# Optimization experiments

Measured on AMD Instinct MI355X. Metric: run time of the kernel, lower is better.

## Reference

```python
import jax, jax.numpy as jnp
import numpy as np

N, E = 50000, 800000
D_IN, H, D_OUT = 64, 64, 32
NEG_SLOPE = 0.2


def setup_inputs() -> dict:
    key = jax.random.key(0)
    ks = jax.random.split(key, 20)
    inp = {
        "x": jax.random.normal(ks[0], (N, D_IN), dtype=jnp.float32),
        "edge_index": jax.random.randint(ks[1], (2, E), 0, N, dtype=jnp.int32),
    }
    def lin(k, fan_in, fan_out):
        s = 1.0 / np.sqrt(fan_in)
        return jax.random.uniform(k, (fan_in, fan_out), jnp.float32, -s, s)
    # GAT layer params: W [in,H], att_src [H], att_dst [H], bias [H]
    dims_in = [D_IN, H, H]
    for i in range(3):
        inp[f"W{i+1}"] = lin(ks[2 + 4 * i], dims_in[i], H)
        inp[f"a_src{i+1}"] = jax.random.normal(ks[3 + 4 * i], (H,), jnp.float32) * 0.1
        inp[f"a_dst{i+1}"] = jax.random.normal(ks[4 + 4 * i], (H,), jnp.float32) * 0.1
        inp[f"b{i+1}"] = jnp.zeros((H,), jnp.float32)
    inp["lin1_W"] = lin(ks[14], H, H)
    inp["lin1_b"] = jnp.zeros((H,), jnp.float32)
    inp["lin2_W"] = lin(ks[15], H, D_OUT)
    inp["lin2_b"] = jnp.zeros((D_OUT,), jnp.float32)
    return inp


def gat_layer(x, src, dst, W, a_src, a_dst, b):
    h = x @ W                                   # [N, H]
    alpha_s = (h * a_src).sum(-1)               # [N]
    alpha_d = (h * a_dst).sum(-1)               # [N]
    e = jax.nn.leaky_relu(alpha_s[src] + alpha_d[dst], NEG_SLOPE)  # [E]
    m = jax.lax.stop_gradient(jax.ops.segment_max(e, dst, num_segments=N))
    w = jnp.exp(e - m[dst])                     # [E]
    denom = jax.ops.segment_sum(w, dst, num_segments=N)
    alpha = w / denom[dst]                      # segment softmax over incoming edges
    out = jax.ops.segment_sum(alpha[:, None] * h[src], dst, num_segments=N)
    return out + b


def reference(x, edge_index, W1, a_src1, a_dst1, b1, W2, a_src2, a_dst2, b2,
              W3, a_src3, a_dst3, b3, lin1_W, lin1_b, lin2_W, lin2_b):
    src, dst = edge_index[0], edge_index[1]
    h = jax.nn.relu(gat_layer(x, src, dst, W1, a_src1, a_dst1, b1))
    h = jax.nn.relu(gat_layer(h, src, dst, W2, a_src2, a_dst2, b2))
    h = jax.nn.relu(gat_layer(h, src, dst, W3, a_src3, a_dst3, b3))
    h = jax.nn.relu(h @ lin1_W + lin1_b)
    return h @ lin2_W + lin2_b
```

## Files before the change

### kernel.cpp

```cpp
#include <hip/hip_runtime.h>

#define NEG_SLOPE 0.2f
#define NBUCK 256

template <bool WANT_ALPHA, bool DO_HIST>
__global__ __launch_bounds__(256) void gemm64(
    const float* __restrict__ x, const float* __restrict__ W,
    const float* __restrict__ a_src, const float* __restrict__ a_dst,
    float* __restrict__ out, float* __restrict__ alpha_s,
    float* __restrict__ alpha_d, int N,
    const int* __restrict__ ei, int E, int* __restrict__ bhist)
{
    __shared__ float Xs[64][68];
    __shared__ float Ws[64][64];
    __shared__ int   hsh[NBUCK];

    const int row0 = blockIdx.x * 64;

    for (int i = threadIdx.x; i < 1024; i += 256)
        ((float4*)Ws)[i] = ((const float4*)W)[i];
    for (int i = threadIdx.x; i < 1024; i += 256) {
        int r = i >> 4, c4 = (i & 15) * 4;
        float4 v = {0.f, 0.f, 0.f, 0.f};
        if (row0 + r < N) v = *(const float4*)&x[(size_t)(row0 + r) * 64 + c4];
        *(float4*)&Xs[r][c4] = v;
    }
    if (DO_HIST && blockIdx.x < 256) hsh[threadIdx.x] = 0;
    __syncthreads();

    const int tx = threadIdx.x & 15;
    const int ty = threadIdx.x >> 4;

    float acc[4][4] = {{0.f,0.f,0.f,0.f},{0.f,0.f,0.f,0.f},
                       {0.f,0.f,0.f,0.f},{0.f,0.f,0.f,0.f}};

#pragma unroll 8
    for (int k = 0; k < 64; ++k) {
        const float4 wv = *(const float4*)&Ws[k][tx * 4];
        const float x0 = Xs[ty * 4 + 0][k];
        const float x1 = Xs[ty * 4 + 1][k];
        const float x2 = Xs[ty * 4 + 2][k];
        const float x3 = Xs[ty * 4 + 3][k];
        acc[0][0] += x0 * wv.x; acc[0][1] += x0 * wv.y;
        acc[0][2] += x0 * wv.z; acc[0][3] += x0 * wv.w;
        acc[1][0] += x1 * wv.x; acc[1][1] += x1 * wv.y;
        acc[1][2] += x1 * wv.z; acc[1][3] += x1 * wv.w;
        acc[2][0] += x2 * wv.x; acc[2][1] += x2 * wv.y;
        acc[2][2] += x2 * wv.z; acc[2][3] += x2 * wv.w;
        acc[3][0] += x3 * wv.x; acc[3][1] += x3 * wv.y;
        acc[3][2] += x3 * wv.z; acc[3][3] += x3 * wv.w;
    }

#pragma unroll
    for (int i = 0; i < 4; ++i) {
        const int r = row0 + ty * 4 + i;
        if (r < N) {
            float4 o = {acc[i][0], acc[i][1], acc[i][2], acc[i][3]};
            *(float4*)&out[(size_t)r * 64 + tx * 4] = o;
        }
    }

    if (WANT_ALPHA) {
        const float4 asv = *(const float4*)&a_src[tx * 4];
        const float4 adv = *(const float4*)&a_dst[tx * 4];
#pragma unroll
        for (int i = 0; i < 4; ++i) {
            float s = acc[i][0]*asv.x + acc[i][1]*asv.y
                    + acc[i][2]*asv.z + acc[i][3]*asv.w;
            float d = acc[i][0]*adv.x + acc[i][1]*adv.y
                    + acc[i][2]*adv.z + acc[i][3]*adv.w;
#pragma unroll
            for (int off = 1; off < 16; off <<= 1) {
                s += __shfl_xor(s, off, 16);
                d += __shfl_xor(d, off, 16);
            }
            const int r = row0 + ty * 4 + i;
            if (tx == 0 && r < N) { alpha_s[r] = s; alpha_d[r] = d; }
        }
    }

    if (DO_HIST && blockIdx.x < 256) {
        __syncthreads();
        for (int e = blockIdx.x * 256 + threadIdx.x; e < E; e += 256 * 256)
            atomicAdd(&hsh[((unsigned)ei[E + e]) >> 8], 1);
        __syncthreads();
        if (hsh[threadIdx.x]) atomicAdd(&bhist[threadIdx.x], hsh[threadIdx.x]);
    }
}

__global__ __launch_bounds__(256) void gemm_head(
    const float* __restrict__ X, const float* __restrict__ W1,
    const float* __restrict__ b1, const float* __restrict__ W2,
    const float* __restrict__ b2, float* __restrict__ out, int N)
{
    __shared__ float Xs[64][68];
    __shared__ float W1s[64][64];
    __shared__ float W2s[64][32];

    const int row0 = blockIdx.x * 64;

    for (int i = threadIdx.x; i < 1024; i += 256)
        ((float4*)W1s)[i] = ((const float4*)W1)[i];
    for (int i = threadIdx.x; i < 512; i += 256)
        ((float4*)W2s)[i] = ((const float4*)W2)[i];
    for (int i = threadIdx.x; i < 1024; i += 256) {
        int r = i >> 4, c4 = (i & 15) * 4;
        float4 v = {0.f, 0.f, 0.f, 0.f};
        if (row0 + r < N) v = *(const float4*)&X[(size_t)(row0 + r) * 64 + c4];
        *(float4*)&Xs[r][c4] = v;
    }
    __syncthreads();

    const int tx = threadIdx.x & 15;
    const int ty = threadIdx.x >> 4;

    float acc[4][4] = {{0,0,0,0},{0,0,0,0},{0,0,0,0},{0,0,0,0}};
#pragma unroll 8
    for (int k = 0; k < 64; ++k) {
        const float4 wv = *(const float4*)&W1s[k][tx * 4];
        const float x0 = Xs[ty * 4 + 0][k];
        const float x1 = Xs[ty * 4 + 1][k];
        const float x2 = Xs[ty * 4 + 2][k];
        const float x3 = Xs[ty * 4 + 3][k];
        acc[0][0] += x0 * wv.x; acc[0][1] += x0 * wv.y;
        acc[0][2] += x0 * wv.z; acc[0][3] += x0 * wv.w;
        acc[1][0] += x1 * wv.x; acc[1][1] += x1 * wv.y;
        acc[1][2] += x1 * wv.z; acc[1][3] += x1 * wv.w;
        acc[2][0] += x2 * wv.x; acc[2][1] += x2 * wv.y;
        acc[2][2] += x2 * wv.z; acc[2][3] += x2 * wv.w;
        acc[3][0] += x3 * wv.x; acc[3][1] += x3 * wv.y;
        acc[3][2] += x3 * wv.z; acc[3][3] += x3 * wv.w;
    }

    const float4 bv = *(const float4*)&b1[tx * 4];
    __syncthreads();
#pragma unroll
    for (int i = 0; i < 4; ++i) {
        Xs[ty * 4 + i][tx * 4 + 0] = fmaxf(acc[i][0] + bv.x, 0.f);
        Xs[ty * 4 + i][tx * 4 + 1] = fmaxf(acc[i][1] + bv.y, 0.f);
        Xs[ty * 4 + i][tx * 4 + 2] = fmaxf(acc[i][2] + bv.z, 0.f);
        Xs[ty * 4 + i][tx * 4 + 3] = fmaxf(acc[i][3] + bv.w, 0.f);
    }
    __syncthreads();

    float a2[4][2] = {{0,0},{0,0},{0,0},{0,0}};
#pragma unroll 8
    for (int k = 0; k < 64; ++k) {
        const float2 wv = *(const float2*)&W2s[k][tx * 2];
        const float t0 = Xs[ty * 4 + 0][k];
        const float t1 = Xs[ty * 4 + 1][k];
        const float t2 = Xs[ty * 4 + 2][k];
        const float t3 = Xs[ty * 4 + 3][k];
        a2[0][0] += t0 * wv.x; a2[0][1] += t0 * wv.y;
        a2[1][0] += t1 * wv.x; a2[1][1] += t1 * wv.y;
        a2[2][0] += t2 * wv.x; a2[2][1] += t2 * wv.y;
        a2[3][0] += t3 * wv.x; a2[3][1] += t3 * wv.y;
    }
    const float2 b2v = *(const float2*)&b2[tx * 2];
#pragma unroll
    for (int i = 0; i < 4; ++i) {
        const int r = row0 + ty * 4 + i;
        if (r < N) {
            float2 o;
            o.x = a2[i][0] + b2v.x;
            o.y = a2[i][1] + b2v.y;
            *(float2*)&out[(size_t)r * 32 + tx * 2] = o;
        }
    }
}

#define PC_EPT 8
#define PC_TILE 2048
__global__ __launch_bounds__(256) void partition_coarse(
    const int* __restrict__ ei, int E, const int* __restrict__ bhist,
    int* __restrict__ gcurs, int* __restrict__ pairs)
{
    __shared__ int sc[NBUCK];
    __shared__ int hist[NBUCK];
    __shared__ int base[NBUCK];
    const int t = threadIdx.x;

    const int bh = bhist[t];
    sc[t] = bh; __syncthreads();
    for (int off = 1; off < 256; off <<= 1) {
        int v = sc[t];
        if (t >= off) v += sc[t - off];
        __syncthreads(); sc[t] = v; __syncthreads();
    }
    const int bbase = sc[t] - bh;
    hist[t] = 0;
    __syncthreads();

    const int tile0 = blockIdx.x * PC_TILE;
    int sv[PC_EPT], dv[PC_EPT], rk[PC_EPT];
#pragma unroll
    for (int i = 0; i < PC_EPT; ++i) {
        const int e = tile0 + i * 256 + t;
        if (e < E) {
            sv[i] = ei[e];
            dv[i] = ei[E + e];
            rk[i] = atomicAdd(&hist[dv[i] >> 8], 1);
        } else dv[i] = -1;
    }
    __syncthreads();
    if (hist[t] > 0) base[t] = bbase + atomicAdd(&gcurs[t], hist[t]);
    __syncthreads();
#pragma unroll
    for (int i = 0; i < PC_EPT; ++i) {
        if (dv[i] >= 0) {
            const int b = dv[i] >> 8;
            pairs[base[b] + rk[i]] = sv[i] | ((dv[i] & 255) << 16);
        }
    }
}

__global__ __launch_bounds__(256) void fine_scatter(
    const int* __restrict__ bhist, const int* __restrict__ pairs,
    int N, int E, int* __restrict__ row_off, int* __restrict__ csr_src)
{
    __shared__ int sc[NBUCK];
    __shared__ int cnt[NBUCK];
    __shared__ int cur[NBUCK];
    const int t = threadIdx.x, b = blockIdx.x;

    const int bh = bhist[t];
    sc[t] = bh; __syncthreads();
    for (int off = 1; off < 256; off <<= 1) {
        int v = sc[t];
        if (t >= off) v += sc[t - off];
        __syncthreads(); sc[t] = v; __syncthreads();
    }
    sc[t] -= bh;
    cnt[t] = 0;
    __syncthreads();

    const int sb = sc[b];
    const int se = sb + bhist[b];

    for (int p = sb + t; p < se; p += 256)
        atomicAdd(&cnt[pairs[p] >> 16], 1);
    __syncthreads();

    const int c = cnt[t];
    cur[t] = c; __syncthreads();
    for (int off = 1; off < 256; off <<= 1) {
        int v = cur[t];
        if (t >= off) v += cur[t - off];
        __syncthreads(); cur[t] = v; __syncthreads();
    }
    const int node_off = sb + cur[t] - c;
    __syncthreads();
    cur[t] = node_off;
    const int n = b * 256 + t;
    if (n < N) row_off[n] = node_off;
    if (b == gridDim.x - 1 && t == 0) row_off[N] = E;
    __syncthreads();

    for (int p = sb + t; p < se; p += 256) {
        const int v = pairs[p];
        const int pos = atomicAdd(&cur[v >> 16], 1);
        csr_src[pos] = v & 0xFFFF;
    }
}

__global__ __launch_bounds__(256) void gat_aggregate(
    const int* __restrict__ row_off, const int* __restrict__ csr_src,
    const float* __restrict__ h, const float* __restrict__ as,
    const float* __restrict__ ad, const float* __restrict__ bias,
    float* __restrict__ out, int N)
{
    const int wv = (blockIdx.x * 256 + threadIdx.x) >> 6;
    if (wv >= N) return;
    const int d    = wv;
    const int lane = threadIdx.x & 63;
    const int g    = lane >> 4;
    const int gl   = lane & 15;

    const int beg = row_off[d], end = row_off[d + 1];
    const float add = ad[d];

    float  den  = 0.f;
    float4 acc0 = {0.f,0.f,0.f,0.f}, acc1 = {0.f,0.f,0.f,0.f};
    float4 acc2 = {0.f,0.f,0.f,0.f}, acc3 = {0.f,0.f,0.f,0.f};

    int s0 = (beg      + g < end) ? csr_src[beg      + g] : 0;
    int s1 = (beg +  4 + g < end) ? csr_src[beg +  4 + g] : 0;
    int s2 = (beg +  8 + g < end) ? csr_src[beg +  8 + g] : 0;
    int s3 = (beg + 12 + g < end) ? csr_src[beg + 12 + g] : 0;

    for (int e0 = beg; e0 < end; e0 += 16) {
        const bool v0 = (e0      + g < end);
        const bool v1 = (e0 +  4 + g < end);
        const bool v2 = (e0 +  8 + g < end);
        const bool v3 = (e0 + 12 + g < end);
        const int cs0 = s0, cs1 = s1, cs2 = s2, cs3 = s3;

        s0 = (e0 + 16 + g < end) ? csr_src[e0 + 16 + g] : 0;
        s1 = (e0 + 20 + g < end) ? csr_src[e0 + 20 + g] : 0;
        s2 = (e0 + 24 + g < end) ? csr_src[e0 + 24 + g] : 0;
        s3 = (e0 + 28 + g < end) ? csr_src[e0 + 28 + g] : 0;

        const float4 h0 = *(const float4*)&h[(size_t)cs0 * 64 + gl * 4];
        const float4 h1 = *(const float4*)&h[(size_t)cs1 * 64 + gl * 4];
        const float4 h2 = *(const float4*)&h[(size_t)cs2 * 64 + gl * 4];
        const float4 h3 = *(const float4*)&h[(size_t)cs3 * 64 + gl * 4];
        const float  a0 = as[cs0];
        const float  a1 = as[cs1];
        const float  a2 = as[cs2];
        const float  a3 = as[cs3];

        float e0v = a0 + add; e0v = (e0v >= 0.f) ? e0v : NEG_SLOPE * e0v;
        float e1v = a1 + add; e1v = (e1v >= 0.f) ? e1v : NEG_SLOPE * e1v;
        float e2v = a2 + add; e2v = (e2v >= 0.f) ? e2v : NEG_SLOPE * e2v;
        float e3v = a3 + add; e3v = (e3v >= 0.f) ? e3v : NEG_SLOPE * e3v;

        const float w0 = v0 ? __expf(e0v) : 0.f;
        const float w1 = v1 ? __expf(e1v) : 0.f;
        const float w2 = v2 ? __expf(e2v) : 0.f;
        const float w3 = v3 ? __expf(e3v) : 0.f;

        den += (w0 + w1) + (w2 + w3);
        acc0.x += w0 * h0.x; acc0.y += w0 * h0.y;
        acc0.z += w0 * h0.z; acc0.w += w0 * h0.w;
        acc1.x += w1 * h1.x; acc1.y += w1 * h1.y;
        acc1.z += w1 * h1.z; acc1.w += w1 * h1.w;
        acc2.x += w2 * h2.x; acc2.y += w2 * h2.y;
        acc2.z += w2 * h2.z; acc2.w += w2 * h2.w;
        acc3.x += w3 * h3.x; acc3.y += w3 * h3.y;
        acc3.z += w3 * h3.z; acc3.w += w3 * h3.w;
    }

    float4 acc;
    acc.x = (acc0.x + acc1.x) + (acc2.x + acc3.x);
    acc.y = (acc0.y + acc1.y) + (acc2.y + acc3.y);
    acc.z = (acc0.z + acc1.z) + (acc2.z + acc3.z);
    acc.w = (acc0.w + acc1.w) + (acc2.w + acc3.w);

#pragma unroll
    for (int off = 16; off <= 32; off <<= 1) {
        acc.x += __shfl_xor(acc.x, off, 64);
        acc.y += __shfl_xor(acc.y, off, 64);
        acc.z += __shfl_xor(acc.z, off, 64);
        acc.w += __shfl_xor(acc.w, off, 64);
        den   += __shfl_xor(den,   off, 64);
    }

    if (g == 0) {
        const float4 bvv = *(const float4*)&bias[gl * 4];
        const float inv = (den > 0.f) ? (1.f / den) : 0.f;
        float4 o;
        o.x = fmaxf(acc.x * inv + bvv.x, 0.f);
        o.y = fmaxf(acc.y * inv + bvv.y, 0.f);
        o.z = fmaxf(acc.z * inv + bvv.z, 0.f);
        o.w = fmaxf(acc.w * inv + bvv.w, 0.f);
        *(float4*)&out[(size_t)d * 64 + gl * 4] = o;
    }
}

extern "C" void kernel_launch(void* const* d_in, const int* in_sizes, int n_in,
                              void* d_out, int out_size, void* d_ws, size_t ws_size,
                              hipStream_t stream)
{
    const float* x  = (const float*)d_in[0];
    const int*   ei = (const int*)d_in[1];
    const float* W[3]    = {(const float*)d_in[2], (const float*)d_in[6],  (const float*)d_in[10]};
    const float* asrc[3] = {(const float*)d_in[3], (const float*)d_in[7],  (const float*)d_in[11]};
    const float* adst[3] = {(const float*)d_in[4], (const float*)d_in[8],  (const float*)d_in[12]};
    const float* bia[3]  = {(const float*)d_in[5], (const float*)d_in[9],  (const float*)d_in[13]};
    const float* lin1W = (const float*)d_in[14];
    const float* lin1b = (const float*)d_in[15];
    const float* lin2W = (const float*)d_in[16];
    const float* lin2b = (const float*)d_in[17];

    const int N = in_sizes[0] / 64;
    const int E = in_sizes[1] / 2;
    const int B = (N + 255) / 256;

    float* X       = (float*)d_ws;
    float* H       = X + (size_t)N * 64;
    float* AS      = H + (size_t)N * 64;
    float* AD      = AS + N;
    int*   row_off = (int*)(AD + N);
    int*   csr_src = row_off + (N + 1);
    int*   bhist   = csr_src + E;
    int*   gcurs   = bhist + 256;
    int*   pairs   = gcurs + 256;

    const int g64_grid = (N + 63) / 64;
    const int agg_grid = (N + 3) / 4;
    const int pc_grid  = (E + PC_TILE - 1) / PC_TILE;

    hipMemsetAsync(bhist, 0, 512 * sizeof(int), stream);

    gemm64<true, true><<<g64_grid, 256, 0, stream>>>(
        x, W[0], asrc[0], adst[0], H, AS, AD, N, ei, E, bhist);

    partition_coarse<<<pc_grid, 256, 0, stream>>>(ei, E, bhist, gcurs, pairs);
    fine_scatter<<<B, 256, 0, stream>>>(bhist, pairs, N, E, row_off, csr_src);

    gat_aggregate<<<agg_grid, 256, 0, stream>>>(
        row_off, csr_src, H, AS, AD, bia[0], X, N);

    for (int l = 1; l < 3; ++l) {
        gemm64<true, false><<<g64_grid, 256, 0, stream>>>(
            X, W[l], asrc[l], adst[l], H, AS, AD, N, nullptr, 0, nullptr);
        gat_aggregate<<<agg_grid, 256, 0, stream>>>(
            row_off, csr_src, H, AS, AD, bia[l], X, N);
    }

    gemm_head<<<g64_grid, 256, 0, stream>>>(
        X, lin1W, lin1b, lin2W, lin2b, (float*)d_out, N);
}
```

Baseline: 202.6 us.

## Fuse GAT aggregation with next layer's GEMM via LDS tiles

Each layer's neighbor aggregation is now done inside the block that runs the following GEMM (or the MLP head). Results go into the shared-memory X tile instead of a global buffer, and the H/alpha buffers ping-pong between layers. This removes the global write and reread of the aggregated features and cuts three kernel launches. In exchange, blocks aggregate 64 destinations with 4 waves, 16 each in sequence, so there are far fewer independent waves than the previous one-wave-per-node aggregation. That may reduce latency hiding for the irregular gathers.

```diff
diff --git a/kernel.cpp b/kernel.cpp
--- a/kernel.cpp
+++ b/kernel.cpp
@@ -3,8 +3,104 @@
 #define NEG_SLOPE 0.2f
 #define NBUCK 256
 
-template <bool WANT_ALPHA, bool DO_HIST>
-__global__ __launch_bounds__(256) void gemm64(
+__device__ __forceinline__ void agg_into_lds(
+    const int* __restrict__ row_off, const int* __restrict__ csr_src,
+    const float* __restrict__ h, const float* __restrict__ as,
+    const float* __restrict__ ad, const float* __restrict__ bias,
+    float (*Xs)[68], int N, int row0)
+{
+    const int lane = threadIdx.x & 63;
+    const int wave = threadIdx.x >> 6;
+    const int g    = lane >> 4;
+    const int gl   = lane & 15;
+
+    const float4 bvv = *(const float4*)&bias[gl * 4];
+
+    for (int it = 0; it < 16; ++it) {
+        const int dl = wave * 16 + it;
+        const int d  = row0 + dl;
+        if (d >= N) break;
+
+        const int beg = row_off[d], end = row_off[d + 1];
+        const float add = ad[d];
+
+        float  den  = 0.f;
+        float4 acc0 = {0.f,0.f,0.f,0.f}, acc1 = {0.f,0.f,0.f,0.f};
+        float4 acc2 = {0.f,0.f,0.f,0.f}, acc3 = {0.f,0.f,0.f,0.f};
+
+        int s0 = (beg      + g < end) ? csr_src[beg      + g] : 0;
+        int s1 = (beg +  4 + g < end) ? csr_src[beg +  4 + g] : 0;
+        int s2 = (beg +  8 + g < end) ? csr_src[beg +  8 + g] : 0;
+        int s3 = (beg + 12 + g < end) ? csr_src[beg + 12 + g] : 0;
+
+        for (int e0 = beg; e0 < end; e0 += 16) {
+            const bool v0 = (e0      + g < end);
+            const bool v1 = (e0 +  4 + g < end);
+            const bool v2 = (e0 +  8 + g < end);
+            const bool v3 = (e0 + 12 + g < end);
+            const int cs0 = s0, cs1 = s1, cs2 = s2, cs3 = s3;
+
+            s0 = (e0 + 16 + g < end) ? csr_src[e0 + 16 + g] : 0;
+            s1 = (e0 + 20 + g < end) ? csr_src[e0 + 20 + g] : 0;
+            s2 = (e0 + 24 + g < end) ? csr_src[e0 + 24 + g] : 0;
+            s3 = (e0 + 28 + g < end) ? csr_src[e0 + 28 + g] : 0;
+
+            const float4 h0 = *(const float4*)&h[(size_t)cs0 * 64 + gl * 4];
+            const float4 h1 = *(const float4*)&h[(size_t)cs1 * 64 + gl * 4];
+            const float4 h2 = *(const float4*)&h[(size_t)cs2 * 64 + gl * 4];
+            const float4 h3 = *(const float4*)&h[(size_t)cs3 * 64 + gl * 4];
+            const float  a0 = as[cs0];
+            const float  a1 = as[cs1];
+            const float  a2 = as[cs2];
+            const float  a3 = as[cs3];
+
+            float e0v = a0 + add; e0v = (e0v >= 0.f) ? e0v : NEG_SLOPE * e0v;
+            float e1v = a1 + add; e1v = (e1v >= 0.f) ? e1v : NEG_SLOPE * e1v;
+            float e2v = a2 + add; e2v = (e2v >= 0.f) ? e2v : NEG_SLOPE * e2v;
+            float e3v = a3 + add; e3v = (e3v >= 0.f) ? e3v : NEG_SLOPE * e3v;
+
+            const float w0 = v0 ? __expf(e0v) : 0.f;
+            const float w1 = v1 ? __expf(e1v) : 0.f;
+            const float w2 = v2 ? __expf(e2v) : 0.f;
+            const float w3 = v3 ? __expf(e3v) : 0.f;
+
+            den += (w0 + w1) + (w2 + w3);
+            acc0.x += w0 * h0.x; acc0.y += w0 * h0.y;
+            acc0.z += w0 * h0.z; acc0.w += w0 * h0.w;
+            acc1.x += w1 * h1.x; acc1.y += w1 * h1.y;
+            acc1.z += w1 * h1.z; acc1.w += w1 * h1.w;
+            acc2.x += w2 * h2.x; acc2.y += w2 * h2.y;
+            acc2.z += w2 * h2.z; acc2.w += w2 * h2.w;
+            acc3.x += w3 * h3.x; acc3.y += w3 * h3.y;
+            acc3.z += w3 * h3.z; acc3.w += w3 * h3.w;
+        }
+
+        float4 acc;
+        acc.x = (acc0.x + acc1.x) + (acc2.x + acc3.x);
+        acc.y = (acc0.y + acc1.y) + (acc2.y + acc3.y);
+        acc.z = (acc0.z + acc1.z) + (acc2.z + acc3.z);
+        acc.w = (acc0.w + acc1.w) + (acc2.w + acc3.w);
+
+#pragma unroll
+        for (int off = 16; off <= 32; off <<= 1) {
+            acc.x += __shfl_xor(acc.x, off, 64);
+            acc.y += __shfl_xor(acc.y, off, 64);
+            acc.z += __shfl_xor(acc.z, off, 64);
+            acc.w += __shfl_xor(acc.w, off, 64);
+            den   += __shfl_xor(den,   off, 64);
+        }
+
+        if (g == 0) {
+            const float inv = (den > 0.f) ? (1.f / den) : 0.f;
+            Xs[dl][gl * 4 + 0] = fmaxf(acc.x * inv + bvv.x, 0.f);
+            Xs[dl][gl * 4 + 1] = fmaxf(acc.y * inv + bvv.y, 0.f);
+            Xs[dl][gl * 4 + 2] = fmaxf(acc.z * inv + bvv.z, 0.f);
+            Xs[dl][gl * 4 + 3] = fmaxf(acc.w * inv + bvv.w, 0.f);
+        }
+    }
+}
+
+__global__ __launch_bounds__(256) void gemm64_l1(
     const float* __restrict__ x, const float* __restrict__ W,
     const float* __restrict__ a_src, const float* __restrict__ a_dst,
     float* __restrict__ out, float* __restrict__ alpha_s,
@@ -25,7 +121,7 @@
         if (row0 + r < N) v = *(const float4*)&x[(size_t)(row0 + r) * 64 + c4];
         *(float4*)&Xs[r][c4] = v;
     }
-    if (DO_HIST && blockIdx.x < 256) hsh[threadIdx.x] = 0;
+    if (blockIdx.x < 256) hsh[threadIdx.x] = 0;
     __syncthreads();
 
     const int tx = threadIdx.x & 15;
@@ -33,7 +129,6 @@
 
     float acc[4][4] = {{0.f,0.f,0.f,0.f},{0.f,0.f,0.f,0.f},
                        {0.f,0.f,0.f,0.f},{0.f,0.f,0.f,0.f}};
-
 #pragma unroll 8
     for (int k = 0; k < 64; ++k) {
         const float4 wv = *(const float4*)&Ws[k][tx * 4];
@@ -60,26 +155,24 @@
         }
     }
 
-    if (WANT_ALPHA) {
-        const float4 asv = *(const float4*)&a_src[tx * 4];
-        const float4 adv = *(const float4*)&a_dst[tx * 4];
-#pragma unroll
-        for (int i = 0; i < 4; ++i) {
-            float s = acc[i][0]*asv.x + acc[i][1]*asv.y
-                    + acc[i][2]*asv.z + acc[i][3]*asv.w;
-            float d = acc[i][0]*adv.x + acc[i][1]*adv.y
-                    + acc[i][2]*adv.z + acc[i][3]*adv.w;
-#pragma unroll
-            for (int off = 1; off < 16; off <<= 1) {
-                s += __shfl_xor(s, off, 16);
-                d += __shfl_xor(d, off, 16);
-            }
-            const int r = row0 + ty * 4 + i;
-            if (tx == 0 && r < N) { alpha_s[r] = s; alpha_d[r] = d; }
-        }
-    }
-
-    if (DO_HIST && blockIdx.x < 256) {
+    const float4 asv = *(const float4*)&a_src[tx * 4];
+    const float4 adv = *(const float4*)&a_dst[tx * 4];
+#pragma unroll
+    for (int i = 0; i < 4; ++i) {
+        float s = acc[i][0]*asv.x + acc[i][1]*asv.y
+                + acc[i][2]*asv.z + acc[i][3]*asv.w;
+        float d = acc[i][0]*adv.x + acc[i][1]*adv.y
+                + acc[i][2]*adv.z + acc[i][3]*adv.w;
+#pragma unroll
+        for (int off = 1; off < 16; off <<= 1) {
+            s += __shfl_xor(s, off, 16);
+            d += __shfl_xor(d, off, 16);
+        }
+        const int r = row0 + ty * 4 + i;
+        if (tx == 0 && r < N) { alpha_s[r] = s; alpha_d[r] = d; }
+    }
+
+    if (blockIdx.x < 256) {
         __syncthreads();
         for (int e = blockIdx.x * 256 + threadIdx.x; e < E; e += 256 * 256)
             atomicAdd(&hsh[((unsigned)ei[E + e]) >> 8], 1);
@@ -88,10 +181,81 @@
     }
 }
 
-__global__ __launch_bounds__(256) void gemm_head(
-    const float* __restrict__ X, const float* __restrict__ W1,
-    const float* __restrict__ b1, const float* __restrict__ W2,
-    const float* __restrict__ b2, float* __restrict__ out, int N)
+__global__ __launch_bounds__(256) void agg_gemm(
+    const int* __restrict__ row_off, const int* __restrict__ csr_src,
+    const float* __restrict__ h_in, const float* __restrict__ as_in,
+    const float* __restrict__ ad_in, const float* __restrict__ bias,
+    const float* __restrict__ W, const float* __restrict__ a_src,
+    const float* __restrict__ a_dst, float* __restrict__ h_out,
+    float* __restrict__ alpha_s, float* __restrict__ alpha_d, int N)
+{
+    __shared__ float Xs[64][68];
+    __shared__ float Ws[64][64];
+
+    const int row0 = blockIdx.x * 64;
+
+    for (int i = threadIdx.x; i < 1024; i += 256)
+        ((float4*)Ws)[i] = ((const float4*)W)[i];
+
+    agg_into_lds(row_off, csr_src, h_in, as_in, ad_in, bias, Xs, N, row0);
+    __syncthreads();
+
+    const int tx = threadIdx.x & 15;
+    const int ty = threadIdx.x >> 4;
+
+    float acc[4][4] = {{0.f,0.f,0.f,0.f},{0.f,0.f,0.f,0.f},
+                       {0.f,0.f,0.f,0.f},{0.f,0.f,0.f,0.f}};
+#pragma unroll 8
+    for (int k = 0; k < 64; ++k) {
+        const float4 wv = *(const float4*)&Ws[k][tx * 4];
+        const float x0 = Xs[ty * 4 + 0][k];
+        const float x1 = Xs[ty * 4 + 1][k];
+        const float x2 = Xs[ty * 4 + 2][k];
+        const float x3 = Xs[ty * 4 + 3][k];
+        acc[0][0] += x0 * wv.x; acc[0][1] += x0 * wv.y;
+        acc[0][2] += x0 * wv.z; acc[0][3] += x0 * wv.w;
+        acc[1][0] += x1 * wv.x; acc[1][1] += x1 * wv.y;
+        acc[1][2] += x1 * wv.z; acc[1][3] += x1 * wv.w;
+        acc[2][0] += x2 * wv.x; acc[2][1] += x2 * wv.y;
+        acc[2][2] += x2 * wv.z; acc[2][3] += x2 * wv.w;
+        acc[3][0] += x3 * wv.x; acc[3][1] += x3 * wv.y;
+        acc[3][2] += x3 * wv.z; acc[3][3] += x3 * wv.w;
+    }
+
+#pragma unroll
+    for (int i = 0; i < 4; ++i) {
+        const int r = row0 + ty * 4 + i;
+        if (r < N) {
+            float4 o = {acc[i][0], acc[i][1], acc[i][2], acc[i][3]};
+            *(float4*)&h_out[(size_t)r * 64 + tx * 4] = o;
+        }
+    }
+
+    const float4 asv = *(const float4*)&a_src[tx * 4];
+    const float4 adv = *(const float4*)&a_dst[tx * 4];
+#pragma unroll
+    for (int i = 0; i < 4; ++i) {
+        float s = acc[i][0]*asv.x + acc[i][1]*asv.y
+                + acc[i][2]*asv.z + acc[i][3]*asv.w;
+        float d = acc[i][0]*adv.x + acc[i][1]*adv.y
+                + acc[i][2]*adv.z + acc[i][3]*adv.w;
+#pragma unroll
+        for (int off = 1; off < 16; off <<= 1) {
+            s += __shfl_xor(s, off, 16);
+            d += __shfl_xor(d, off, 16);
+        }
+        const int r = row0 + ty * 4 + i;
+        if (tx == 0 && r < N) { alpha_s[r] = s; alpha_d[r] = d; }
+    }
+}
+
+__global__ __launch_bounds__(256) void agg_head(
+    const int* __restrict__ row_off, const int* __restrict__ csr_src,
+    const float* __restrict__ h_in, const float* __restrict__ as_in,
+    const float* __restrict__ ad_in, const float* __restrict__ bias,
+    const float* __restrict__ W1, const float* __restrict__ b1,
+    const float* __restrict__ W2, const float* __restrict__ b2,
+    float* __restrict__ out, int N)
 {
     __shared__ float Xs[64][68];
     __shared__ float W1s[64][64];
@@ -103,12 +267,8 @@
         ((float4*)W1s)[i] = ((const float4*)W1)[i];
     for (int i = threadIdx.x; i < 512; i += 256)
         ((float4*)W2s)[i] = ((const float4*)W2)[i];
-    for (int i = threadIdx.x; i < 1024; i += 256) {
-        int r = i >> 4, c4 = (i & 15) * 4;
-        float4 v = {0.f, 0.f, 0.f, 0.f};
-        if (row0 + r < N) v = *(const float4*)&X[(size_t)(row0 + r) * 64 + c4];
-        *(float4*)&Xs[r][c4] = v;
-    }
+
+    agg_into_lds(row_off, csr_src, h_in, as_in, ad_in, bias, Xs, N, row0);
     __syncthreads();
 
     const int tx = threadIdx.x & 15;
@@ -161,9 +321,7 @@
     for (int i = 0; i < 4; ++i) {
         const int r = row0 + ty * 4 + i;
         if (r < N) {
-            float2 o;
-            o.x = a2[i][0] + b2v.x;
-            o.y = a2[i][1] + b2v.y;
+            float2 o = {a2[i][0] + b2v.x, a2[i][1] + b2v.y};
             *(float2*)&out[(size_t)r * 32 + tx * 2] = o;
         }
     }
@@ -260,100 +418,6 @@
         const int v = pairs[p];
         const int pos = atomicAdd(&cur[v >> 16], 1);
         csr_src[pos] = v & 0xFFFF;
-    }
-}
-
-__global__ __launch_bounds__(256) void gat_aggregate(
-    const int* __restrict__ row_off, const int* __restrict__ csr_src,
-    const float* __restrict__ h, const float* __restrict__ as,
-    const float* __restrict__ ad, const float* __restrict__ bias,
-    float* __restrict__ out, int N)
-{
-    const int wv = (blockIdx.x * 256 + threadIdx.x) >> 6;
-    if (wv >= N) return;
-    const int d    = wv;
-    const int lane = threadIdx.x & 63;
-    const int g    = lane >> 4;
-    const int gl   = lane & 15;
-
-    const int beg = row_off[d], end = row_off[d + 1];
-    const float add = ad[d];
-
-    float  den  = 0.f;
-    float4 acc0 = {0.f,0.f,0.f,0.f}, acc1 = {0.f,0.f,0.f,0.f};
-    float4 acc2 = {0.f,0.f,0.f,0.f}, acc3 = {0.f,0.f,0.f,0.f};
-
-    int s0 = (beg      + g < end) ? csr_src[beg      + g] : 0;
-    int s1 = (beg +  4 + g < end) ? csr_src[beg +  4 + g] : 0;
-    int s2 = (beg +  8 + g < end) ? csr_src[beg +  8 + g] : 0;
-    int s3 = (beg + 12 + g < end) ? csr_src[beg + 12 + g] : 0;
-
-    for (int e0 = beg; e0 < end; e0 += 16) {
-        const bool v0 = (e0      + g < end);
-        const bool v1 = (e0 +  4 + g < end);
-        const bool v2 = (e0 +  8 + g < end);
-        const bool v3 = (e0 + 12 + g < end);
-        const int cs0 = s0, cs1 = s1, cs2 = s2, cs3 = s3;
-
-        s0 = (e0 + 16 + g < end) ? csr_src[e0 + 16 + g] : 0;
-        s1 = (e0 + 20 + g < end) ? csr_src[e0 + 20 + g] : 0;
-        s2 = (e0 + 24 + g < end) ? csr_src[e0 + 24 + g] : 0;
-        s3 = (e0 + 28 + g < end) ? csr_src[e0 + 28 + g] : 0;
-
-        const float4 h0 = *(const float4*)&h[(size_t)cs0 * 64 + gl * 4];
-        const float4 h1 = *(const float4*)&h[(size_t)cs1 * 64 + gl * 4];
-        const float4 h2 = *(const float4*)&h[(size_t)cs2 * 64 + gl * 4];
-        const float4 h3 = *(const float4*)&h[(size_t)cs3 * 64 + gl * 4];
-        const float  a0 = as[cs0];
-        const float  a1 = as[cs1];
-        const float  a2 = as[cs2];
-        const float  a3 = as[cs3];
-
-        float e0v = a0 + add; e0v = (e0v >= 0.f) ? e0v : NEG_SLOPE * e0v;
-        float e1v = a1 + add; e1v = (e1v >= 0.f) ? e1v : NEG_SLOPE * e1v;
-        float e2v = a2 + add; e2v = (e2v >= 0.f) ? e2v : NEG_SLOPE * e2v;
-        float e3v = a3 + add; e3v = (e3v >= 0.f) ? e3v : NEG_SLOPE * e3v;
-
-        const float w0 = v0 ? __expf(e0v) : 0.f;
-        const float w1 = v1 ? __expf(e1v) : 0.f;
-        const float w2 = v2 ? __expf(e2v) : 0.f;
-        const float w3 = v3 ? __expf(e3v) : 0.f;
-
-        den += (w0 + w1) + (w2 + w3);
-        acc0.x += w0 * h0.x; acc0.y += w0 * h0.y;
-        acc0.z += w0 * h0.z; acc0.w += w0 * h0.w;
-        acc1.x += w1 * h1.x; acc1.y += w1 * h1.y;
-        acc1.z += w1 * h1.z; acc1.w += w1 * h1.w;
-        acc2.x += w2 * h2.x; acc2.y += w2 * h2.y;
-        acc2.z += w2 * h2.z; acc2.w += w2 * h2.w;
-        acc3.x += w3 * h3.x; acc3.y += w3 * h3.y;
-        acc3.z += w3 * h3.z; acc3.w += w3 * h3.w;
-    }
-
-    float4 acc;
-    acc.x = (acc0.x + acc1.x) + (acc2.x + acc3.x);
-    acc.y = (acc0.y + acc1.y) + (acc2.y + acc3.y);
-    acc.z = (acc0.z + acc1.z) + (acc2.z + acc3.z);
-    acc.w = (acc0.w + acc1.w) + (acc2.w + acc3.w);
-
-#pragma unroll
-    for (int off = 16; off <= 32; off <<= 1) {
-        acc.x += __shfl_xor(acc.x, off, 64);
-        acc.y += __shfl_xor(acc.y, off, 64);
-        acc.z += __shfl_xor(acc.z, off, 64);
-        acc.w += __shfl_xor(acc.w, off, 64);
-        den   += __shfl_xor(den,   off, 64);
-    }
-
-    if (g == 0) {
-        const float4 bvv = *(const float4*)&bias[gl * 4];
-        const float inv = (den > 0.f) ? (1.f / den) : 0.f;
-        float4 o;
-        o.x = fmaxf(acc.x * inv + bvv.x, 0.f);
-        o.y = fmaxf(acc.y * inv + bvv.y, 0.f);
-        o.z = fmaxf(acc.z * inv + bvv.z, 0.f);
-        o.w = fmaxf(acc.w * inv + bvv.w, 0.f);
-        *(float4*)&out[(size_t)d * 64 + gl * 4] = o;
     }
 }
 
@@ -376,38 +440,38 @@
     const int E = in_sizes[1] / 2;
     const int B = (N + 255) / 256;
 
-    float* X       = (float*)d_ws;
-    float* H       = X + (size_t)N * 64;
-    float* AS      = H + (size_t)N * 64;
-    float* AD      = AS + N;
-    int*   row_off = (int*)(AD + N);
+    float* Ha      = (float*)d_ws;
+    float* Hb      = Ha + (size_t)N * 64;
+    float* ASa     = Hb + (size_t)N * 64;
+    float* ADa     = ASa + N;
+    float* ASb     = ADa + N;
+    float* ADb     = ASb + N;
+    int*   row_off = (int*)(ADb + N);
     int*   csr_src = row_off + (N + 1);
     int*   bhist   = csr_src + E;
     int*   gcurs   = bhist + 256;
     int*   pairs   = gcurs + 256;
 
     const int g64_grid = (N + 63) / 64;
-    const int agg_grid = (N + 3) / 4;
     const int pc_grid  = (E + PC_TILE - 1) / PC_TILE;
 
     hipMemsetAsync(bhist, 0, 512 * sizeof(int), stream);
 
-    gemm64<true, true><<<g64_grid, 256, 0, stream>>>(
-        x, W[0], asrc[0], adst[0], H, AS, AD, N, ei, E, bhist);
+    gemm64_l1<<<g64_grid, 256, 0, stream>>>(
+        x, W[0], asrc[0], adst[0], Ha, ASa, ADa, N, ei, E, bhist);
 
     partition_coarse<<<pc_grid, 256, 0, stream>>>(ei, E, bhist, gcurs, pairs);
     fine_scatter<<<B, 256, 0, stream>>>(bhist, pairs, N, E, row_off, csr_src);
 
-    gat_aggregate<<<agg_grid, 256, 0, stream>>>(
-        row_off, csr_src, H, AS, AD, bia[0], X, N);
-
-    for (int l = 1; l < 3; ++l) {
-        gemm64<true, false><<<g64_grid, 256, 0, stream>>>(
-            X, W[l], asrc[l], adst[l], H, AS, AD, N, nullptr, 0, nullptr);
-        gat_aggregate<<<agg_grid, 256, 0, stream>>>(
-            row_off, csr_src, H, AS, AD, bia[l], X, N);
-    }
-
-    gemm_head<<<g64_grid, 256, 0, stream>>>(
-        X, lin1W, lin1b, lin2W, lin2b, (float*)d_out, N);
-}
+    agg_gemm<<<g64_grid, 256, 0, stream>>>(
+        row_off, csr_src, Ha, ASa, ADa, bia[0],
+        W[1], asrc[1], adst[1], Hb, ASb, ADb, N);
+
+    agg_gemm<<<g64_grid, 256, 0, stream>>>(
+        row_off, csr_src, Hb, ASb, ADb, bia[1],
+        W[2], asrc[2], adst[2], Ha, ASa, ADa, N);
+
+    agg_head<<<g64_grid, 256, 0, stream>>>(
+        row_off, csr_src, Ha, ASa, ADa, bia[2],
+        lin1W, lin1b, lin2W, lin2b, (float*)d_out, N);
+}
```

New measurement: 229.8 us. +13.4%, slower.
